# Optimization experiments

Measured on AMD Instinct MI355X. Metric: run time of the kernel, lower is better.

Reference implementation:

```python
import jax, jax.numpy as jnp
import numpy as np

N, G, H1, H2, HEADS, EMB, C, S = 4096, 2048, 512, 128, 8, 16, 20, 4
CH = H1 // HEADS  # per-head channels = 64
EPS = 1e-6
COEF_FE = 0.1


def _uni(k, shape, fan_in, fan_out):
    c = np.sqrt(6.0 / (fan_in + fan_out)).astype(np.float32)
    return jax.random.uniform(k, shape, jnp.float32, -c, c)


def setup_inputs() -> dict:
    key = jax.random.key(0)
    ks = jax.random.split(key, 40)
    adj = (jax.random.uniform(ks[0], (N, N)) < 0.005).astype(jnp.float32)
    adj = jnp.maximum(adj, jnp.eye(N, dtype=jnp.float32))  # self-loops, no empty rows
    node_feats = jax.random.normal(ks[1], (N, G), jnp.float32)
    count_matrix = jax.random.randint(ks[2], (N, G), 0, 50).astype(jnp.float32)
    library_size = jax.random.uniform(ks[3], (N, 1), jnp.float32, 0.5, 2.0)
    slice_label = jax.random.randint(ks[4], (N,), 0, S)
    basis = jax.random.uniform(ks[5], (C, G), jnp.float32)
    # encoder GAT layer1: HEADS heads, c_in=G -> c_out=CH each
    We1 = _uni(ks[6], (HEADS, CH, G), G, CH)
    be1 = jnp.zeros((HEADS, CH), jnp.float32)
    v0e1 = _uni(ks[7], (HEADS, CH, 1), CH, 1)
    v1e1 = _uni(ks[8], (HEADS, CH, 1), CH, 1)
    # encoder dense layer2: H1 -> H2
    W2 = _uni(ks[9], (H2, H1), H1, H2)
    b2 = jnp.zeros((H2,), jnp.float32)
    # decoder GAT layer1: c_in = H2+EMB -> CH per head
    CIN_D = H2 + EMB
    Wd1 = _uni(ks[10], (HEADS, CH, CIN_D), CIN_D, CH)
    bd1 = jnp.zeros((HEADS, CH), jnp.float32)
    v0d1 = _uni(ks[11], (HEADS, CH, 1), CH, 1)
    v1d1 = _uni(ks[12], (HEADS, CH, 1), CH, 1)
    # decoder dense layer2: H1 -> G
    Wd2 = _uni(ks[13], (G, H1), H1, G)
    bd2 = jnp.zeros((G,), jnp.float32)
    # deconv alpha (H2+EMB -> 1) and beta (H2 -> C); zero-init in torch, small random here
    Wa = 0.01 * jax.random.normal(ks[14], (1, CIN_D), jnp.float32)
    ba = jnp.zeros((1,), jnp.float32)
    Wb = 0.01 * jax.random.normal(ks[15], (C, H2), jnp.float32)
    bb = jnp.zeros((C,), jnp.float32)
    gamma = 0.01 * jax.random.normal(ks[16], (S, G), jnp.float32)
    logtheta = 5.0 * jnp.ones((S, G), jnp.float32)
    emb_table = jax.random.normal(ks[17], (S, EMB), jnp.float32)
    return dict(adj_matrix=adj, node_feats=node_feats, count_matrix=count_matrix,
                library_size=library_size, slice_label=slice_label, basis=basis,
                We1=We1, be1=be1, v0e1=v0e1, v1e1=v1e1, W2=W2, b2=b2,
                Wd1=Wd1, bd1=bd1, v0d1=v0d1, v1d1=v1d1, Wd2=Wd2, bd2=bd2,
                Wa=Wa, ba=ba, Wb=Wb, bb=bb, gamma=gamma, logtheta=logtheta,
                emb_table=emb_table)


def _gat_head(x, adj, W, b, v0, v1):
    h = x @ W.T + b                       # [N, CH]
    logits = adj * ((h @ v0) + (h @ v1).T)  # [N, N]; zero where adj==0
    s = jax.nn.sigmoid(logits) - 0.5       # unnormalized attentions
    mask = adj != 0.0
    e = jnp.where(mask, jnp.exp(s), 0.0)    # sparse softmax over structural nonzeros (temp=1)
    den = e.sum(axis=1, keepdims=True)
    p = e / jnp.where(den == 0.0, 1.0, den)
    return p @ h                            # [N, CH]


def _gat_multi(x, adj, Ws, bs, v0s, v1s):
    return jnp.concatenate([_gat_head(x, adj, Ws[i], bs[i], v0s[i], v1s[i])
                            for i in range(HEADS)], axis=1)


def reference(adj_matrix, node_feats, count_matrix, library_size, slice_label, basis,
              We1, be1, v0e1, v1e1, W2, b2, Wd1, bd1, v0d1, v1d1, Wd2, bd2,
              Wa, ba, Wb, bb, gamma, logtheta, emb_table):
    # encoder
    H = jax.nn.elu(_gat_multi(node_feats, adj_matrix, We1, be1, v0e1, v1e1))
    Z = H @ W2.T + b2                                   # [N, H2]
    emb = emb_table[slice_label]                        # [N, EMB]
    # deconvolutioner
    beta = jax.nn.softmax(jax.nn.elu(Z) @ Wb.T + bb, axis=1)   # [N, C]
    Hc = jax.nn.elu(jnp.concatenate([Z, emb], axis=1))
    alpha = Hc @ Wa.T + ba                              # [N, 1]
    # decoder
    Hd = jax.nn.elu(_gat_multi(jnp.concatenate([Z, emb], axis=1), adj_matrix,
                               Wd1, bd1, v0d1, v1d1))
    X_recon = Hd @ Wd2.T + bd2                          # [N, G]
    features_loss = jnp.mean(jnp.sqrt(jnp.sum((node_feats - X_recon) ** 2, axis=1)))
    # NB deconvolution loss
    log_lam = jnp.log(beta @ basis + EPS) + alpha + gamma[slice_label]
    lam = jnp.exp(log_lam)
    th = jnp.exp(logtheta)[slice_label]                 # [N, G]
    mu = library_size * lam
    ll = (jax.lax.lgamma(count_matrix + th + EPS) - jax.lax.lgamma(th + EPS)
          + th * jnp.log(th + EPS) - th * jnp.log(th + mu + EPS)
          + count_matrix * jnp.log(mu + EPS) - count_matrix * jnp.log(th + mu + EPS))
    decon_loss = -jnp.mean(jnp.sum(ll, axis=1))
    return decon_loss + COEF_FE * features_loss
```

## Files before the change

kernel.cpp:

```cpp
#include <hip/hip_runtime.h>
#include <hip/hip_bf16.h>
#include <math.h>

#define N 4096
#define G 2048
#define H1 512
#define H2 128
#define HEADS 8
#define EMB 16
#define C 20
#define S 4
#define CH 64
#define CIN_D (H2 + EMB)
#define KD_PAD 160
#define KB_PAD 32
#define CAP 128
#define EPSV 1e-6f

typedef __attribute__((ext_vector_type(8))) short short8;
typedef __attribute__((ext_vector_type(8))) short bf16x8;
typedef __attribute__((ext_vector_type(4))) float f32x4;

__device__ __forceinline__ unsigned short f2b(float x) {
    __hip_bfloat16 h = __float2bfloat16(x);
    return *reinterpret_cast<unsigned short*>(&h);
}
__device__ __forceinline__ float b2f(unsigned short u) {
    unsigned int x = ((unsigned int)u) << 16;
    return __uint_as_float(x);
}
__device__ __forceinline__ float lgamma_fast(float x) {
    float sh = 0.f;
    while (x < 8.f) { sh -= __logf(x); x += 1.f; }
    float ix = 1.f / x;
    float lx = __logf(x);
    return (x - 0.5f) * lx - x + 0.91893853f
         + ix * (0.08333333f - 0.00277778f * ix * ix) + sh;
}

#define SEG_SG   (S * G)
#define SEG_NF4  (N * G / 4)
#define SEG_WE4  (H1 * G / 4)
#define SEG_W24  (H2 * H1 / 4)
#define SEG_WD1E (H1 * KD_PAD)
#define SEG_WD24 (G * H1 / 4)
#define SEG_BTE  (G * KB_PAD)
#define PREP_TOTAL (SEG_SG + SEG_NF4 + SEG_WE4 + SEG_W24 + SEG_WD1E + SEG_WD24 + SEG_BTE)
#define CSR_BLOCKS (N / 4)
#define PREP_BLOCKS ((PREP_TOTAL + 255) / 256)

__device__ __forceinline__ void cvt4(const float* __restrict__ in,
                                     unsigned short* __restrict__ out, int i) {
    float4 v = ((const float4*)in)[i];
    ushort4 o;
    o.x = f2b(v.x); o.y = f2b(v.y); o.z = f2b(v.z); o.w = f2b(v.w);
    ((ushort4*)out)[i] = o;
}

__global__ __launch_bounds__(256) void csr_prep(const float* __restrict__ adj,
                                                int* __restrict__ col_idx,
                                                int* __restrict__ row_cnt,
                                                const float* __restrict__ logtheta,
                                                const float* __restrict__ gamma,
                                                float* __restrict__ th_a, float* __restrict__ eg_a,
                                                float* __restrict__ gm_a, float* __restrict__ ax_a,
                                                const float* __restrict__ node_f,
                                                unsigned short* __restrict__ nf_bf,
                                                const float* __restrict__ We1,
                                                unsigned short* __restrict__ We1_bf,
                                                const float* __restrict__ W2,
                                                unsigned short* __restrict__ W2_bf,
                                                const float* __restrict__ Wd1,
                                                unsigned short* __restrict__ Wd1_bf,
                                                const float* __restrict__ Wd2,
                                                unsigned short* __restrict__ Wd2_bf,
                                                const float* __restrict__ basis,
                                                unsigned short* __restrict__ basisT_bf) {
    int b = blockIdx.x;
    if (b < CSR_BLOCKS) {
        int wv = threadIdx.x >> 6, lane = threadIdx.x & 63;
        int i = b * 4 + wv;
        int cnt = 0;
        const float4* row4 = (const float4*)(adj + (size_t)i * N);
        int* cols = col_idx + (size_t)i * CAP;
        unsigned long long lmask = (1ull << lane) - 1ull;
        for (int c = 0; c < N / 256; ++c) {
            float4 v = row4[c * 64 + lane];
            float vv[4] = {v.x, v.y, v.z, v.w};
            #pragma unroll
            for (int s = 0; s < 4; ++s) {
                unsigned long long m = __ballot(vv[s] != 0.f);
                if (vv[s] != 0.f) {
                    int idx = cnt + __popcll(m & lmask);
                    if (idx < CAP) cols[idx] = c * 256 + lane * 4 + s;
                }
                cnt += __popcll(m);
            }
        }
        if (lane == 0) row_cnt[i] = cnt < CAP ? cnt : CAP;
        return;
    }
    int idx = (b - CSR_BLOCKS) * 256 + threadIdx.x;
    if (idx < SEG_SG) {
        float th = __expf(logtheta[idx]);
        float gm = gamma[idx];
        th_a[idx] = th;
        eg_a[idx] = __expf(gm);
        gm_a[idx] = gm;
        ax_a[idx] = th * __logf(th + EPSV) - lgammaf(th + EPSV);
        return;
    }
    idx -= SEG_SG;
    if (idx < SEG_NF4) { cvt4(node_f, nf_bf, idx); return; }
    idx -= SEG_NF4;
    if (idx < SEG_WE4) { cvt4(We1, We1_bf, idx); return; }
    idx -= SEG_WE4;
    if (idx < SEG_W24) { cvt4(W2, W2_bf, idx); return; }
    idx -= SEG_W24;
    if (idx < SEG_WD1E) {
        int n = idx / KD_PAD, k = idx - n * KD_PAD;
        Wd1_bf[idx] = f2b(k < CIN_D ? Wd1[n * CIN_D + k] : 0.f);
        return;
    }
    idx -= SEG_WD1E;
    if (idx < SEG_WD24) { cvt4(Wd2, Wd2_bf, idx); return; }
    idx -= SEG_WD24;
    if (idx < SEG_BTE) {
        int g = idx >> 5, c = idx & 31;
        basisT_bf[idx] = f2b(c < C ? basis[c * G + g] : 0.f);
    }
}

#define LDP 40
template<int FM, int OBF, int KS, int HV>
__global__ __launch_bounds__(256) void gemm_mfma(const unsigned short* __restrict__ A,
                                                 const unsigned short* __restrict__ B,
                                                 const float* __restrict__ bias,
                                                 void* __restrict__ Cout,
                                                 int M, int Nc, int K,
                                                 const float* __restrict__ v0f,
                                                 const float* __restrict__ v1f,
                                                 float* __restrict__ hv0,
                                                 float* __restrict__ hv1) {
    constexpr int BMT = FM * 32;
    __shared__ short As[BMT * LDP];
    __shared__ short Bs[128 * LDP];
    int bn = blockIdx.x, bm = blockIdx.y;
    int kz = (KS > 1) ? blockIdx.z : 0;
    int t = threadIdx.x;
    int lane = t & 63, wid = t >> 6;
    int wr = wid >> 1, wc = wid & 1;
    f32x4 acc[FM][4] = {};
    const short* Ag = (const short*)A + (size_t)(bm * BMT) * K;
    const short* Bg = (const short*)B + (size_t)(bn * 128) * K;
    int r0 = t >> 2, q0 = t & 3;
    int rbase = (lane & 15);
    int koff = (lane >> 4) * 8;
    int kbeg = kz * (K / KS), kend = kbeg + K / KS;

    for (int k0 = kbeg; k0 < kend; k0 += 32) {
        short8 a0 = *(const short8*)(Ag + (size_t)r0 * K + k0 + q0 * 8);
        short8 a1;
        if constexpr (FM == 4) a1 = *(const short8*)(Ag + (size_t)(r0 + 64) * K + k0 + q0 * 8);
        short8 b0 = *(const short8*)(Bg + (size_t)r0 * K + k0 + q0 * 8);
        short8 b1 = *(const short8*)(Bg + (size_t)(r0 + 64) * K + k0 + q0 * 8);
        __syncthreads();
        *(short8*)(As + r0 * LDP + q0 * 8) = a0;
        if constexpr (FM == 4) *(short8*)(As + (r0 + 64) * LDP + q0 * 8) = a1;
        *(short8*)(Bs + r0 * LDP + q0 * 8) = b0;
        *(short8*)(Bs + (r0 + 64) * LDP + q0 * 8) = b1;
        __syncthreads();
        bf16x8 af[FM], bfr[4];
        #pragma unroll
        for (int m = 0; m < FM; ++m)
            af[m] = *(const bf16x8*)(As + (wr * FM * 16 + m * 16 + rbase) * LDP + koff);
        #pragma unroll
        for (int n = 0; n < 4; ++n)
            bfr[n] = *(const bf16x8*)(Bs + (wc * 64 + n * 16 + rbase) * LDP + koff);
        #pragma unroll
        for (int m = 0; m < FM; ++m)
            #pragma unroll
            for (int n = 0; n < 4; ++n)
                acc[m][n] = __builtin_amdgcn_mfma_f32_16x16x32_bf16(af[m], bfr[n], acc[m][n], 0, 0, 0);
    }
    int colb = bn * 128 + wc * 64;
    int rowb = bm * BMT + wr * FM * 16;
    #pragma unroll
    for (int m = 0; m < FM; ++m) {
        #pragma unroll
        for (int n = 0; n < 4; ++n) {
            int col = colb + n * 16 + (lane & 15);
            int row0 = rowb + m * 16 + (lane >> 4) * 4;
            if constexpr (KS > 1) {
                float* Cp = (float*)Cout + (size_t)kz * M * Nc;
                #pragma unroll
                for (int r = 0; r < 4; ++r)
                    Cp[(size_t)(row0 + r) * Nc + col] = acc[m][n][r];
            } else {
                float bs = bias ? bias[col] : 0.f;
                #pragma unroll
                for (int r = 0; r < 4; ++r) {
                    float v = acc[m][n][r] + bs;
                    if constexpr (OBF)
                        ((unsigned short*)Cout)[(size_t)(row0 + r) * Nc + col] = f2b(v);
                    else
                        ((float*)Cout)[(size_t)(row0 + r) * Nc + col] = v;
                }
            }
        }
    }
    if constexpr (HV) {
        int h = colb >> 6;
        #pragma unroll
        for (int m = 0; m < FM; ++m) {
            #pragma unroll
            for (int r = 0; r < 4; ++r) {
                int row = rowb + m * 16 + (lane >> 4) * 4 + r;
                float p0 = 0.f, p1 = 0.f;
                #pragma unroll
                for (int n = 0; n < 4; ++n) {
                    int col = colb + n * 16 + (lane & 15);
                    float v = acc[m][n][r] + bias[col];
                    p0 += v * v0f[col];
                    p1 += v * v1f[col];
                }
                p0 += __shfl_xor(p0, 1); p0 += __shfl_xor(p0, 2);
                p0 += __shfl_xor(p0, 4); p0 += __shfl_xor(p0, 8);
                p1 += __shfl_xor(p1, 1); p1 += __shfl_xor(p1, 2);
                p1 += __shfl_xor(p1, 4); p1 += __shfl_xor(p1, 8);
                if ((lane & 15) == 0) {
                    hv0[row * HEADS + h] = p0;
                    hv1[row * HEADS + h] = p1;
                }
            }
        }
    }
}

template<int HV>
__device__ __forceinline__ void gemm_body2(const unsigned short* __restrict__ A,
                                           const unsigned short* __restrict__ B,
                                           const float* __restrict__ bias,
                                           unsigned short* __restrict__ Cout,
                                           int K, int Nc, int bn, int bm,
                                           const float* __restrict__ v0f,
                                           const float* __restrict__ v1f,
                                           float* __restrict__ hv0,
                                           float* __restrict__ hv1,
                                           short* As, short* Bs) {
    int t = threadIdx.x;
    int lane = t & 63, wid = t >> 6;
    int wr = wid >> 1, wc = wid & 1;
    f32x4 acc[2][4] = {};
    const short* Ag = (const short*)A + (size_t)(bm * 64) * K;
    const short* Bg = (const short*)B + (size_t)(bn * 128) * K;
    int r0 = t >> 2, q0 = t & 3;
    int rbase = (lane & 15);
    int koff = (lane >> 4) * 8;
    for (int k0 = 0; k0 < K; k0 += 32) {
        short8 a0 = *(const short8*)(Ag + (size_t)r0 * K + k0 + q0 * 8);
        short8 b0 = *(const short8*)(Bg + (size_t)r0 * K + k0 + q0 * 8);
        short8 b1 = *(const short8*)(Bg + (size_t)(r0 + 64) * K + k0 + q0 * 8);
        __syncthreads();
        *(short8*)(As + r0 * LDP + q0 * 8) = a0;
        *(short8*)(Bs + r0 * LDP + q0 * 8) = b0;
        *(short8*)(Bs + (r0 + 64) * LDP + q0 * 8) = b1;
        __syncthreads();
        bf16x8 af[2], bfr[4];
        #pragma unroll
        for (int m = 0; m < 2; ++m)
            af[m] = *(const bf16x8*)(As + (wr * 32 + m * 16 + rbase) * LDP + koff);
        #pragma unroll
        for (int n = 0; n < 4; ++n)
            bfr[n] = *(const bf16x8*)(Bs + (wc * 64 + n * 16 + rbase) * LDP + koff);
        #pragma unroll
        for (int m = 0; m < 2; ++m)
            #pragma unroll
            for (int n = 0; n < 4; ++n)
                acc[m][n] = __builtin_amdgcn_mfma_f32_16x16x32_bf16(af[m], bfr[n], acc[m][n], 0, 0, 0);
    }
    int colb = bn * 128 + wc * 64;
    int rowb = bm * 64 + wr * 32;
    #pragma unroll
    for (int m = 0; m < 2; ++m) {
        #pragma unroll
        for (int n = 0; n < 4; ++n) {
            int col = colb + n * 16 + (lane & 15);
            int row0 = rowb + m * 16 + (lane >> 4) * 4;
            float bs = bias ? bias[col] : 0.f;
            #pragma unroll
            for (int r = 0; r < 4; ++r)
                Cout[(size_t)(row0 + r) * Nc + col] = f2b(acc[m][n][r] + bs);
        }
    }
    if constexpr (HV) {
        int h = colb >> 6;
        #pragma unroll
        for (int m = 0; m < 2; ++m) {
            #pragma unroll
            for (int r = 0; r < 4; ++r) {
                int row = rowb + m * 16 + (lane >> 4) * 4 + r;
                float p0 = 0.f, p1 = 0.f;
                #pragma unroll
                for (int n = 0; n < 4; ++n) {
                    int col = colb + n * 16 + (lane & 15);
                    float v = acc[m][n][r] + bias[col];
                    p0 += v * v0f[col];
                    p1 += v * v1f[col];
                }
                p0 += __shfl_xor(p0, 1); p0 += __shfl_xor(p0, 2);
                p0 += __shfl_xor(p0, 4); p0 += __shfl_xor(p0, 8);
                p1 += __shfl_xor(p1, 1); p1 += __shfl_xor(p1, 2);
                p1 += __shfl_xor(p1, 4); p1 += __shfl_xor(p1, 8);
                if ((lane & 15) == 0) {
                    hv0[row * HEADS + h] = p0;
                    hv1[row * HEADS + h] = p1;
                }
            }
        }
    }
}

__global__ __launch_bounds__(256) void dec_bd(const unsigned short* __restrict__ Xd_bf,
                                              const unsigned short* __restrict__ Wd1_bf,
                                              const float* __restrict__ bd1,
                                              unsigned short* __restrict__ Hlin_bf,
                                              const float* __restrict__ v0d1,
                                              const float* __restrict__ v1d1,
                                              float* __restrict__ hv0,
                                              float* __restrict__ hv1,
                                              const unsigned short* __restrict__ beta_bf,
                                              const unsigned short* __restrict__ basisT_bf,
                                              unsigned short* __restrict__ BDb) {
    __shared__ short As[64 * LDP];
    __shared__ short Bs[128 * LDP];
    int b = blockIdx.x;
    if (b < (H1 / 128) * (N / 64)) {
        gemm_body2<1>(Xd_bf, Wd1_bf, bd1, Hlin_bf, KD_PAD, H1,
                      b % (H1 / 128), b / (H1 / 128), v0d1, v1d1, hv0, hv1, As, Bs);
    } else {
        int b2 = b - (H1 / 128) * (N / 64);
        gemm_body2<0>(beta_bf, basisT_bf, nullptr, BDb, KB_PAD, G,
                      b2 % (G / 128), b2 / (G / 128), nullptr, nullptr, nullptr, nullptr, As, Bs);
    }
}

template<int KS>
__global__ __launch_bounds__(256) void reduce_k_hv(const float* __restrict__ Cp,
                                                   const float* __restrict__ bias,
                                                   unsigned short* __restrict__ out,
                                                   const float* __restrict__ v0f,
                                                   const float* __restrict__ v1f,
                                                   float* __restrict__ hv0,
                                                   float* __restrict__ hv1) {
    constexpr int total4 = N * H1 / 4;
    int t = threadIdx.x;
    int i = blockIdx.x * 256 + t;
    float4 s = ((const float4*)Cp)[i];
    #pragma unroll
    for (int ks = 1; ks < KS; ++ks) {
        float4 v = ((const float4*)(Cp + (size_t)ks * total4 * 4))[i];
        s.x += v.x; s.y += v.y; s.z += v.z; s.w += v.w;
    }
    int col = (i * 4) & (H1 - 1);
    s.x += bias[col]; s.y += bias[col + 1]; s.z += bias[col + 2]; s.w += bias[col + 3];
    ushort4 o;
    o.x = f2b(s.x); o.y = f2b(s.y); o.z = f2b(s.z); o.w = f2b(s.w);
    ((ushort4*)out)[i] = o;
    int row = (i * 4) >> 9;
    int h = col >> 6;
    float4 w0 = *(const float4*)(v0f + col);
    float4 w1 = *(const float4*)(v1f + col);
    float p0 = s.x * w0.x + s.y * w0.y + s.z * w0.z + s.w * w0.w;
    float p1 = s.x * w1.x + s.y * w1.y + s.z * w1.z + s.w * w1.w;
    p0 += __shfl_xor(p0, 1); p0 += __shfl_xor(p0, 2);
    p0 += __shfl_xor(p0, 4); p0 += __shfl_xor(p0, 8);
    p1 += __shfl_xor(p1, 1); p1 += __shfl_xor(p1, 2);
    p1 += __shfl_xor(p1, 4); p1 += __shfl_xor(p1, 8);
    if ((t & 15) == 0) {
        hv0[row * HEADS + h] = p0;
        hv1[row * HEADS + h] = p1;
    }
}

__global__ __launch_bounds__(256) void z_pernode(const float* __restrict__ Cp,
                                                 const float* __restrict__ b2,
                                                 const float* __restrict__ emb_table,
                                                 const int* __restrict__ slab,
                                                 const float* __restrict__ Wb,
                                                 const float* __restrict__ bb,
                                                 const float* __restrict__ Wa,
                                                 const float* __restrict__ ba,
                                                 const float* __restrict__ lib,
                                                 unsigned short* __restrict__ beta_bf,
                                                 float* __restrict__ muf,
                                                 float* __restrict__ kco,
                                                 unsigned short* __restrict__ Xdb) {
    __shared__ float sZ[4][H2];
    __shared__ float sE[4][EMB];
    __shared__ float sLog[4][C];
    __shared__ float sAl[4];
    int wv = threadIdx.x >> 6;
    int lane = threadIdx.x & 63;
    int i = blockIdx.x * 4 + wv;
    float z0 = 0.f, z1 = 0.f;
    #pragma unroll
    for (int ks = 0; ks < 8; ++ks) {
        const float* P = Cp + (size_t)ks * N * H2 + (size_t)i * H2;
        z0 += P[lane];
        z1 += P[64 + lane];
    }
    z0 += b2[lane];
    z1 += b2[64 + lane];
    sZ[wv][lane] = z0;
    sZ[wv][64 + lane] = z1;
    int s = slab[i];
    if (lane < EMB) sE[wv][lane] = emb_table[s * EMB + lane];
    __syncthreads();
    Xdb[(size_t)i * KD_PAD + lane] = f2b(z0);
    Xdb[(size_t)i * KD_PAD + 64 + lane] = f2b(z1);
    if (lane < EMB) Xdb[(size_t)i * KD_PAD + H2 + lane] = f2b(sE[wv][lane]);
    if (lane < KD_PAD - CIN_D) Xdb[(size_t)i * KD_PAD + CIN_D + lane] = 0;
    if (lane < C) {
        float acc = bb[lane];
        for (int k = 0; k < H2; ++k) {
            float z = sZ[wv][k];
            float e = z > 0.f ? z : expm1f(z);
            acc += e * Wb[lane * H2 + k];
        }
        sLog[wv][lane] = acc;
    }
    __syncthreads();
    if (lane == 0) {
        float mx = sLog[wv][0];
        for (int c = 1; c < C; ++c) mx = fmaxf(mx, sLog[wv][c]);
        float sm = 0.f;
        for (int c = 0; c < C; ++c) { float e = __expf(sLog[wv][c] - mx); sLog[wv][c] = e; sm += e; }
        for (int c = 0; c < C; ++c) sLog[wv][c] /= sm;
    }
    __syncthreads();
    if (lane < KB_PAD) beta_bf[(size_t)i * KB_PAD + lane] = (lane < C) ? f2b(sLog[wv][lane]) : 0;
    float x0 = z0; x0 = x0 > 0.f ? x0 : expm1f(x0);
    float x1 = z1; x1 = x1 > 0.f ? x1 : expm1f(x1);
    float p = x0 * Wa[lane] + x1 * Wa[64 + lane];
    if (lane < EMB) {
        float x2 = sE[wv][lane]; x2 = x2 > 0.f ? x2 : expm1f(x2);
        p += x2 * Wa[H2 + lane];
    }
    #pragma unroll
    for (int m = 32; m; m >>= 1) p += __shfl_xor(p, m);
    if (lane == 0) sAl[wv] = p + ba[0];
    __syncthreads();
    if (lane == 0) {
        float A = sAl[wv], L = lib[i];
        muf[i] = L * __expf(A);
        kco[i] = __logf(L) + A;
    }
}

__global__ __launch_bounds__(256) void gemm_recon_sq(const unsigned short* __restrict__ A,
                                                     const unsigned short* __restrict__ B,
                                                     const float* __restrict__ bias,
                                                     const unsigned short* __restrict__ nfb,
                                                     float* __restrict__ sq_part) {
    constexpr int K = H1;
    __shared__ short As[64 * LDP];
    __shared__ short Bs[128 * LDP];
    __shared__ float red[4][32];
    int bn = blockIdx.x, bm = blockIdx.y;
    int t = threadIdx.x;
    int lane = t & 63, wid = t >> 6;
    int wr = wid >> 1, wc = wid & 1;
    f32x4 acc[2][4] = {};
    const short* Ag = (const short*)A + (size_t)(bm * 64) * K;
    const short* Bg = (const short*)B + (size_t)(bn * 128) * K;
    int r0 = t >> 2, q0 = t & 3;
    int rbase = (lane & 15);
    int koff = (lane >> 4) * 8;

    for (int k0 = 0; k0 < K; k0 += 32) {
        short8 a0 = *(const short8*)(Ag + (size_t)r0 * K + k0 + q0 * 8);
        short8 b0 = *(const short8*)(Bg + (size_t)r0 * K + k0 + q0 * 8);
        short8 b1 = *(const short8*)(Bg + (size_t)(r0 + 64) * K + k0 + q0 * 8);
        __syncthreads();
        *(short8*)(As + r0 * LDP + q0 * 8) = a0;
        *(short8*)(Bs + r0 * LDP + q0 * 8) = b0;
        *(short8*)(Bs + (r0 + 64) * LDP + q0 * 8) = b1;
        __syncthreads();
        bf16x8 af[2], bfr[4];
        #pragma unroll
        for (int m = 0; m < 2; ++m)
            af[m] = *(const bf16x8*)(As + (wr * 32 + m * 16 + rbase) * LDP + koff);
        #pragma unroll
        for (int n = 0; n < 4; ++n)
            bfr[n] = *(const bf16x8*)(Bs + (wc * 64 + n * 16 + rbase) * LDP + koff);
        #pragma unroll
        for (int m = 0; m < 2; ++m)
            #pragma unroll
            for (int n = 0; n < 4; ++n)
                acc[m][n] = __builtin_amdgcn_mfma_f32_16x16x32_bf16(af[m], bfr[n], acc[m][n], 0, 0, 0);
    }
    int colb = bn * 128 + wc * 64;
    int rowb = bm * 64 + wr * 32;
    float part[2][4];
    #pragma unroll
    for (int m = 0; m < 2; ++m) {
        #pragma unroll
        for (int r = 0; r < 4; ++r) part[m][r] = 0.f;
        #pragma unroll
        for (int n = 0; n < 4; ++n) {
            int col = colb + n * 16 + (lane & 15);
            float bs = bias[col];
            int row0 = rowb + m * 16 + (lane >> 4) * 4;
            #pragma unroll
            for (int r = 0; r < 4; ++r) {
                float d = b2f(nfb[(size_t)(row0 + r) * G + col]) - (acc[m][n][r] + bs);
                part[m][r] += d * d;
            }
        }
    }
    #pragma unroll
    for (int m = 0; m < 2; ++m)
        #pragma unroll
        for (int r = 0; r < 4; ++r) {
            float v = part[m][r];
            v += __shfl_xor(v, 1); v += __shfl_xor(v, 2);
            v += __shfl_xor(v, 4); v += __shfl_xor(v, 8);
            part[m][r] = v;
        }
    if ((lane & 15) == 0) {
        int q = lane >> 4;
        #pragma unroll
        for (int m = 0; m < 2; ++m)
            #pragma unroll
            for (int r = 0; r < 4; ++r)
                red[wid][m * 16 + q * 4 + r] = part[m][r];
    }
    __syncthreads();
    if (t < 64) {
        int wr2 = t >> 5, loc = t & 31;
        float v = red[wr2 * 2 + 0][loc] + red[wr2 * 2 + 1][loc];
        sq_part[(size_t)(bm * 64 + t) * 16 + bn] = v;
    }
}

__global__ __launch_bounds__(256) void nb_loss_ew(const unsigned short* __restrict__ BDb,
                                                  const float* __restrict__ cm,
                                                  const int* __restrict__ slab,
                                                  const float* __restrict__ muf,
                                                  const float* __restrict__ kco,
                                                  const float* __restrict__ th_a,
                                                  const float* __restrict__ eg_a,
                                                  const float* __restrict__ gm_a,
                                                  const float* __restrict__ ax_a,
                                                  float* __restrict__ ll_row) {
    int row = blockIdx.x * 4 + (threadIdx.x >> 6);
    int lane = threadIdx.x & 63;
    int sl = slab[row];
    float mufv = muf[row], kcov = kco[row];
    const unsigned short* bdr = BDb + (size_t)row * G;
    const float* cmr = cm + (size_t)row * G;
    size_t sgb = (size_t)sl * G;
    float acc = 0.f;
    #pragma unroll 2
    for (int it = 0; it < G / 256; ++it) {
        int c = it * 256 + lane * 4;
        ushort4 bdu = *(const ushort4*)(bdr + c);
        f32x4 k4  = *(const f32x4*)(cmr + c);
        f32x4 th4 = *(const f32x4*)(th_a + sgb + c);
        f32x4 eg4 = *(const f32x4*)(eg_a + sgb + c);
        f32x4 gm4 = *(const f32x4*)(gm_a + sgb + c);
        f32x4 ax4 = *(const f32x4*)(ax_a + sgb + c);
        float bdv[4] = {b2f(bdu.x), b2f(bdu.y), b2f(bdu.z), b2f(bdu.w)};
        #pragma unroll
        for (int j = 0; j < 4; ++j) {
            float th = th4[j], k = k4[j];
            float ebd = bdv[j] + EPSV;
            float lbd = __logf(ebd);
            float mu = mufv * ebd * eg4[j];
            float lgx = lgamma_fast(k + th + EPSV);
            acc += lgx + ax4[j] - (th + k) * __logf(th + mu + EPSV)
                 + k * (kcov + lbd + gm4[j]);
        }
    }
    #pragma unroll
    for (int m = 32; m; m >>= 1) acc += __shfl_xor(acc, m);
    if (lane == 0) ll_row[row] = acc;
}

__global__ __launch_bounds__(512) void attn_fused(const unsigned short* __restrict__ Hb,
                                                  const float* __restrict__ hv0,
                                                  const float* __restrict__ hv1,
                                                  const int* __restrict__ col_idx,
                                                  const int* __restrict__ row_cnt,
                                                  unsigned short* __restrict__ out) {
    __shared__ int scols[CAP];
    __shared__ float sw[CAP][HEADS];
    __shared__ float sden[HEADS];
    __shared__ float red[8][64 * 8];
    int i = blockIdx.x;
    int t = threadIdx.x;
    int cnt = row_cnt[i];
    const int* cols = col_idx + (size_t)i * CAP;
    if (t < cnt) scols[t] = cols[t];
    __syncthreads();
    for (int idx = t; idx < cnt * HEADS; idx += 512) {
        int e = idx >> 3, h = idx & 7;
        int j = scols[e];
        float x = hv0[i * HEADS + h] + hv1[j * HEADS + h];
        sw[e][h] = __expf(1.f / (1.f + __expf(-x)) - 0.5f);
    }
    __syncthreads();
    if (t < HEADS) {
        float d = 0.f;
        for (int e = 0; e < cnt; ++e) d += sw[e][t];
        sden[t] = 1.f / d;
    }
    __syncthreads();
    int slot = t >> 6;
    int cg = t & 63;
    int h = cg >> 3;
    float inv = sden[h];
    float acc[8];
    #pragma unroll
    for (int k = 0; k < 8; ++k) acc[k] = 0.f;
    for (int e = slot; e < cnt; e += 8) {
        int j = scols[e];
        float wv = sw[e][h] * inv;
        short8 hv = ((const short8*)(Hb + (size_t)j * H1))[cg];
        #pragma unroll
        for (int k = 0; k < 8; ++k)
            acc[k] += wv * b2f((unsigned short)hv[k]);
    }
    #pragma unroll
    for (int k = 0; k < 8; ++k) red[slot][cg * 8 + k] = acc[k];
    __syncthreads();
    if (slot < 4) {
        #pragma unroll
        for (int k = 0; k < 8; ++k) red[slot][cg * 8 + k] += red[slot + 4][cg * 8 + k];
    }
    __syncthreads();
    if (slot < 2) {
        #pragma unroll
        for (int k = 0; k < 8; ++k) red[slot][cg * 8 + k] += red[slot + 2][cg * 8 + k];
    }
    __syncthreads();
    if (slot == 0) {
        short8 o;
        #pragma unroll
        for (int k = 0; k < 8; ++k) {
            float v = red[0][cg * 8 + k] + red[1][cg * 8 + k];
            v = (v > 0.f) ? v : expm1f(v);
            o[k] = (short)f2b(v);
        }
        ((short8*)(out + (size_t)i * H1))[cg] = o;
    }
}

__global__ __launch_bounds__(256) void final_reduce(const float* __restrict__ ll_row,
                                                    const float* __restrict__ sq_part,
                                                    float* __restrict__ out) {
    int t = threadIdx.x;
    float s1 = 0.f, sb = 0.f;
    for (int row = t; row < N; row += 256) {
        s1 += ll_row[row];
        float s2 = 0.f;
        #pragma unroll
        for (int j = 0; j < 16; ++j) s2 += sq_part[(size_t)row * 16 + j];
        sb += sqrtf(s2);
    }
    __shared__ float r1[256], r2[256];
    r1[t] = s1; r2[t] = sb;
    __syncthreads();
    for (int o = 128; o; o >>= 1) {
        if (t < o) { r1[t] += r1[t + o]; r2[t] += r2[t + o]; }
        __syncthreads();
    }
    if (t == 0) out[0] = -(r1[0] / (float)N) + 0.1f * (r2[0] / (float)N);
}

extern "C" void kernel_launch(void* const* d_in, const int* in_sizes, int n_in,
                              void* d_out, int out_size, void* d_ws, size_t ws_size,
                              hipStream_t stream) {
    const float* adj       = (const float*)d_in[0];
    const float* node_f    = (const float*)d_in[1];
    const float* count_m   = (const float*)d_in[2];
    const float* lib       = (const float*)d_in[3];
    const int*   slab      = (const int*)d_in[4];
    const float* basis     = (const float*)d_in[5];
    const float* We1       = (const float*)d_in[6];
    const float* be1       = (const float*)d_in[7];
    const float* v0e1      = (const float*)d_in[8];
    const float* v1e1      = (const float*)d_in[9];
    const float* W2        = (const float*)d_in[10];
    const float* b2        = (const float*)d_in[11];
    const float* Wd1       = (const float*)d_in[12];
    const float* bd1       = (const float*)d_in[13];
    const float* v0d1      = (const float*)d_in[14];
    const float* v1d1      = (const float*)d_in[15];
    const float* Wd2       = (const float*)d_in[16];
    const float* bd2       = (const float*)d_in[17];
    const float* Wa        = (const float*)d_in[18];
    const float* ba        = (const float*)d_in[19];
    const float* Wb        = (const float*)d_in[20];
    const float* bb        = (const float*)d_in[21];
    const float* gamma     = (const float*)d_in[22];
    const float* logtheta  = (const float*)d_in[23];
    const float* emb_table = (const float*)d_in[24];
    float* out = (float*)d_out;

    char* w = (char*)d_ws;
    auto alloc = [&](size_t bytes) { void* p = (void*)w; w += (bytes + 255) & ~(size_t)255; return p; };
    int*   col_idx = (int*)  alloc((size_t)N * CAP * 4);
    int*   row_cnt = (int*)  alloc((size_t)N * 4);
    unsigned short* Hlin_bf = (unsigned short*)alloc((size_t)N * H1 * 2);
    unsigned short* Hgat_bf = (unsigned short*)alloc((size_t)N * H1 * 2);
    unsigned short* Xd_bf   = (unsigned short*)alloc((size_t)N * KD_PAD * 2);
    unsigned short* beta_bf = (unsigned short*)alloc((size_t)N * KB_PAD * 2);
    float* muf     = (float*)alloc((size_t)N * 4);
    float* kco     = (float*)alloc((size_t)N * 4);
    float* hv0     = (float*)alloc((size_t)N * HEADS * 4);
    float* hv1     = (float*)alloc((size_t)N * HEADS * 4);
    float* th_a    = (float*)alloc((size_t)S * G * 4);
    float* eg_a    = (float*)alloc((size_t)S * G * 4);
    float* gm_a    = (float*)alloc((size_t)S * G * 4);
    float* ax_a    = (float*)alloc((size_t)S * G * 4);
    float* Cp      = (float*)alloc((size_t)4 * N * H1 * 4);
    unsigned short* BDb = (unsigned short*)alloc((size_t)N * G * 2);
    float* ll_row  = (float*)alloc((size_t)N * 4);
    float* sq_part = (float*)alloc((size_t)N * 16 * 4);
    unsigned short* nf_bf    = (unsigned short*)alloc((size_t)N * G * 2);
    unsigned short* We1_bf   = (unsigned short*)alloc((size_t)H1 * G * 2);
    unsigned short* W2_bf    = (unsigned short*)alloc((size_t)H2 * H1 * 2);
    unsigned short* Wd1_bf   = (unsigned short*)alloc((size_t)H1 * KD_PAD * 2);
    unsigned short* Wd2_bf   = (unsigned short*)alloc((size_t)G * H1 * 2);
    unsigned short* basisT_bf= (unsigned short*)alloc((size_t)G * KB_PAD * 2);

    csr_prep<<<dim3(CSR_BLOCKS + PREP_BLOCKS), dim3(256), 0, stream>>>(
        adj, col_idx, row_cnt, logtheta, gamma, th_a, eg_a, gm_a, ax_a,
        node_f, nf_bf, We1, We1_bf, W2, W2_bf, Wd1, Wd1_bf, Wd2, Wd2_bf, basis, basisT_bf);

    gemm_mfma<2, 0, 4, 0><<<dim3(H1 / 128, N / 64, 4), dim3(256), 0, stream>>>(
        nf_bf, We1_bf, be1, Cp, N, H1, G, nullptr, nullptr, nullptr, nullptr);
    reduce_k_hv<4><<<dim3(N * H1 / 4 / 256), dim3(256), 0, stream>>>(
        Cp, be1, Hlin_bf, v0e1, v1e1, hv0, hv1);
    attn_fused<<<dim3(N), dim3(512), 0, stream>>>(Hlin_bf, hv0, hv1, col_idx, row_cnt, Hgat_bf);
    gemm_mfma<2, 0, 8, 0><<<dim3(H2 / 128, N / 64, 8), dim3(256), 0, stream>>>(
        Hgat_bf, W2_bf, b2, Cp, N, H2, H1, nullptr, nullptr, nullptr, nullptr);
    z_pernode<<<dim3(N / 4), dim3(256), 0, stream>>>(
        Cp, b2, emb_table, slab, Wb, bb, Wa, ba, lib, beta_bf, muf, kco, Xd_bf);
    dec_bd<<<dim3((H1 / 128) * (N / 64) + (G / 128) * (N / 64)), dim3(256), 0, stream>>>(
        Xd_bf, Wd1_bf, bd1, Hlin_bf, v0d1, v1d1, hv0, hv1, beta_bf, basisT_bf, BDb);
    nb_loss_ew<<<dim3(N / 4), dim3(256), 0, stream>>>(
        BDb, count_m, slab, muf, kco, th_a, eg_a, gm_a, ax_a, ll_row);
    attn_fused<<<dim3(N), dim3(512), 0, stream>>>(Hlin_bf, hv0, hv1, col_idx, row_cnt, Hgat_bf);
    gemm_recon_sq<<<dim3(G / 128, N / 64), dim3(256), 0, stream>>>(
        Hgat_bf, Wd2_bf, bd2, nf_bf, sq_part);
    final_reduce<<<dim3(1), dim3(256), 0, stream>>>(ll_row, sq_part, out);
}
```

Measured before the change: 185.7 us.

## Fuse decoder attention with NB loss kernel and rewrite CSR extraction

Merges the second attention kernel and the NB loss elementwise kernel into one launch, with block ranges split between the two independent workloads so they run concurrently and one launch is saved. The CSR build now has each lane scan a contiguous 64-column chunk into a bitmask, then uses a wave prefix scan to place column indices. This replaces the per-element ballot loop. The cost is that the NB blocks now run 512 threads each while also carrying the attention kernel's shared-memory footprint, which may lower occupancy. The new CSR reads are strided per lane, which may hurt load coalescing.

```diff
diff --git a/kernel.cpp b/kernel.cpp
--- a/kernel.cpp
+++ b/kernel.cpp
@@ -80,24 +80,34 @@
     if (b < CSR_BLOCKS) {
         int wv = threadIdx.x >> 6, lane = threadIdx.x & 63;
         int i = b * 4 + wv;
-        int cnt = 0;
         const float4* row4 = (const float4*)(adj + (size_t)i * N);
+        unsigned long long mask = 0ull;
+        #pragma unroll
+        for (int q = 0; q < 16; ++q) {
+            float4 v = row4[lane * 16 + q];
+            if (v.x != 0.f) mask |= 1ull << (q * 4 + 0);
+            if (v.y != 0.f) mask |= 1ull << (q * 4 + 1);
+            if (v.z != 0.f) mask |= 1ull << (q * 4 + 2);
+            if (v.w != 0.f) mask |= 1ull << (q * 4 + 3);
+        }
+        int cnt = __popcll(mask);
+        int incl = cnt;
+        #pragma unroll
+        for (int off = 1; off < 64; off <<= 1) {
+            int v = __shfl_up(incl, off);
+            if (lane >= off) incl += v;
+        }
+        int ofs = incl - cnt;
+        int total = __shfl(incl, 63);
         int* cols = col_idx + (size_t)i * CAP;
-        unsigned long long lmask = (1ull << lane) - 1ull;
-        for (int c = 0; c < N / 256; ++c) {
-            float4 v = row4[c * 64 + lane];
-            float vv[4] = {v.x, v.y, v.z, v.w};
-            #pragma unroll
-            for (int s = 0; s < 4; ++s) {
-                unsigned long long m = __ballot(vv[s] != 0.f);
-                if (vv[s] != 0.f) {
-                    int idx = cnt + __popcll(m & lmask);
-                    if (idx < CAP) cols[idx] = c * 256 + lane * 4 + s;
-                }
-                cnt += __popcll(m);
-            }
-        }
-        if (lane == 0) row_cnt[i] = cnt < CAP ? cnt : CAP;
+        unsigned long long mm = mask;
+        while (mm) {
+            int j = __ffsll(mm) - 1;
+            if (ofs < CAP) cols[ofs] = lane * 64 + j;
+            ++ofs;
+            mm &= mm - 1;
+        }
+        if (lane == 0) row_cnt[i] = total < CAP ? total : CAP;
         return;
     }
     int idx = (b - CSR_BLOCKS) * 256 + threadIdx.x;
@@ -544,18 +554,17 @@
     }
 }
 
-__global__ __launch_bounds__(256) void nb_loss_ew(const unsigned short* __restrict__ BDb,
-                                                  const float* __restrict__ cm,
-                                                  const int* __restrict__ slab,
-                                                  const float* __restrict__ muf,
-                                                  const float* __restrict__ kco,
-                                                  const float* __restrict__ th_a,
-                                                  const float* __restrict__ eg_a,
-                                                  const float* __restrict__ gm_a,
-                                                  const float* __restrict__ ax_a,
-                                                  float* __restrict__ ll_row) {
-    int row = blockIdx.x * 4 + (threadIdx.x >> 6);
-    int lane = threadIdx.x & 63;
+__device__ __forceinline__ void nb_row_body(int row, int lane,
+                                            const unsigned short* __restrict__ BDb,
+                                            const float* __restrict__ cm,
+                                            const int* __restrict__ slab,
+                                            const float* __restrict__ muf,
+                                            const float* __restrict__ kco,
+                                            const float* __restrict__ th_a,
+                                            const float* __restrict__ eg_a,
+                                            const float* __restrict__ gm_a,
+                                            const float* __restrict__ ax_a,
+                                            float* __restrict__ ll_row) {
     int sl = slab[row];
     float mufv = muf[row], kcov = kco[row];
     const unsigned short* bdr = BDb + (size_t)row * G;
@@ -588,72 +597,106 @@
     if (lane == 0) ll_row[row] = acc;
 }
 
+__device__ __forceinline__ void attn_body(int i, int t,
+                                          const unsigned short* __restrict__ Hb,
+                                          const float* __restrict__ hv0,
+                                          const float* __restrict__ hv1,
+                                          const int* __restrict__ col_idx,
+                                          const int* __restrict__ row_cnt,
+                                          unsigned short* __restrict__ outp) {
+    __shared__ int scols[CAP];
+    __shared__ float sw[CAP][HEADS];
+    __shared__ float sden[HEADS];
+    __shared__ float red[8][64 * 8];
+    int cnt = row_cnt[i];
+    const int* cols = col_idx + (size_t)i * CAP;
+    if (t < cnt) scols[t] = cols[t];
+    __syncthreads();
+    for (int idx = t; idx < cnt * HEADS; idx += 512) {
+        int e = idx >> 3, h = idx & 7;
+        int j = scols[e];
+        float x = hv0[i * HEADS + h] + hv1[j * HEADS + h];
+        sw[e][h] = __expf(1.f / (1.f + __expf(-x)) - 0.5f);
+    }
+    __syncthreads();
+    if (t < HEADS) {
+        float d = 0.f;
+        for (int e = 0; e < cnt; ++e) d += sw[e][t];
+        sden[t] = 1.f / d;
+    }
+    __syncthreads();
+    int slot = t >> 6;
+    int cg = t & 63;
+    int h = cg >> 3;
+    float inv = sden[h];
+    float acc[8];
+    #pragma unroll
+    for (int k = 0; k < 8; ++k) acc[k] = 0.f;
+    for (int e = slot; e < cnt; e += 8) {
+        int j = scols[e];
+        float wv = sw[e][h] * inv;
+        short8 hvv = ((const short8*)(Hb + (size_t)j * H1))[cg];
+        #pragma unroll
+        for (int k = 0; k < 8; ++k)
+            acc[k] += wv * b2f((unsigned short)hvv[k]);
+    }
+    #pragma unroll
+    for (int k = 0; k < 8; ++k) red[slot][cg * 8 + k] = acc[k];
+    __syncthreads();
+    if (slot < 4) {
+        #pragma unroll
+        for (int k = 0; k < 8; ++k) red[slot][cg * 8 + k] += red[slot + 4][cg * 8 + k];
+    }
+    __syncthreads();
+    if (slot < 2) {
+        #pragma unroll
+        for (int k = 0; k < 8; ++k) red[slot][cg * 8 + k] += red[slot + 2][cg * 8 + k];
+    }
+    __syncthreads();
+    if (slot == 0) {
+        short8 o;
+        #pragma unroll
+        for (int k = 0; k < 8; ++k) {
+            float v = red[0][cg * 8 + k] + red[1][cg * 8 + k];
+            v = (v > 0.f) ? v : expm1f(v);
+            o[k] = (short)f2b(v);
+        }
+        ((short8*)(outp + (size_t)i * H1))[cg] = o;
+    }
+}
+
 __global__ __launch_bounds__(512) void attn_fused(const unsigned short* __restrict__ Hb,
                                                   const float* __restrict__ hv0,
                                                   const float* __restrict__ hv1,
                                                   const int* __restrict__ col_idx,
                                                   const int* __restrict__ row_cnt,
                                                   unsigned short* __restrict__ out) {
-    __shared__ int scols[CAP];
-    __shared__ float sw[CAP][HEADS];
-    __shared__ float sden[HEADS];
-    __shared__ float red[8][64 * 8];
-    int i = blockIdx.x;
-    int t = threadIdx.x;
-    int cnt = row_cnt[i];
-    const int* cols = col_idx + (size_t)i * CAP;
-    if (t < cnt) scols[t] = cols[t];
-    __syncthreads();
-    for (int idx = t; idx < cnt * HEADS; idx += 512) {
-        int e = idx >> 3, h = idx & 7;
-        int j = scols[e];
-        float x = hv0[i * HEADS + h] + hv1[j * HEADS + h];
-        sw[e][h] = __expf(1.f / (1.f + __expf(-x)) - 0.5f);
-    }
-    __syncthreads();
-    if (t < HEADS) {
-        float d = 0.f;
-        for (int e = 0; e < cnt; ++e) d += sw[e][t];
-        sden[t] = 1.f / d;
-    }
-    __syncthreads();
-    int slot = t >> 6;
-    int cg = t & 63;
-    int h = cg >> 3;
-    float inv = sden[h];
-    float acc[8];
-    #pragma unroll
-    for (int k = 0; k < 8; ++k) acc[k] = 0.f;
-    for (int e = slot; e < cnt; e += 8) {
-        int j = scols[e];
-        float wv = sw[e][h] * inv;
-        short8 hv = ((const short8*)(Hb + (size_t)j * H1))[cg];
-        #pragma unroll
-        for (int k = 0; k < 8; ++k)
-            acc[k] += wv * b2f((unsigned short)hv[k]);
-    }
-    #pragma unroll
-    for (int k = 0; k < 8; ++k) red[slot][cg * 8 + k] = acc[k];
-    __syncthreads();
-    if (slot < 4) {
-        #pragma unroll
-        for (int k = 0; k < 8; ++k) red[slot][cg * 8 + k] += red[slot + 4][cg * 8 + k];
-    }
-    __syncthreads();
-    if (slot < 2) {
-        #pragma unroll
-        for (int k = 0; k < 8; ++k) red[slot][cg * 8 + k] += red[slot + 2][cg * 8 + k];
-    }
-    __syncthreads();
-    if (slot == 0) {
-        short8 o;
-        #pragma unroll
-        for (int k = 0; k < 8; ++k) {
-            float v = red[0][cg * 8 + k] + red[1][cg * 8 + k];
-            v = (v > 0.f) ? v : expm1f(v);
-            o[k] = (short)f2b(v);
-        }
-        ((short8*)(out + (size_t)i * H1))[cg] = o;
+    attn_body(blockIdx.x, threadIdx.x, Hb, hv0, hv1, col_idx, row_cnt, out);
+}
+
+__global__ __launch_bounds__(512) void post_dec(const unsigned short* __restrict__ Hlin_bf,
+                                                const float* __restrict__ hv0,
+                                                const float* __restrict__ hv1,
+                                                const int* __restrict__ col_idx,
+                                                const int* __restrict__ row_cnt,
+                                                unsigned short* __restrict__ Hgat_bf,
+                                                const unsigned short* __restrict__ BDb,
+                                                const float* __restrict__ cm,
+                                                const int* __restrict__ slab,
+                                                const float* __restrict__ muf,
+                                                const float* __restrict__ kco,
+                                                const float* __restrict__ th_a,
+                                                const float* __restrict__ eg_a,
+                                                const float* __restrict__ gm_a,
+                                                const float* __restrict__ ax_a,
+                                                float* __restrict__ ll_row) {
+    int b = blockIdx.x;
+    if (b < N) {
+        attn_body(b, threadIdx.x, Hlin_bf, hv0, hv1, col_idx, row_cnt, Hgat_bf);
+    } else {
+        int row = (b - N) * 8 + (threadIdx.x >> 6);
+        nb_row_body(row, threadIdx.x & 63, BDb, cm, slab, muf, kco,
+                    th_a, eg_a, gm_a, ax_a, ll_row);
     }
 }
 
@@ -751,9 +794,9 @@
         Cp, b2, emb_table, slab, Wb, bb, Wa, ba, lib, beta_bf, muf, kco, Xd_bf);
     dec_bd<<<dim3((H1 / 128) * (N / 64) + (G / 128) * (N / 64)), dim3(256), 0, stream>>>(
         Xd_bf, Wd1_bf, bd1, Hlin_bf, v0d1, v1d1, hv0, hv1, beta_bf, basisT_bf, BDb);
-    nb_loss_ew<<<dim3(N / 4), dim3(256), 0, stream>>>(
+    post_dec<<<dim3(N + N / 8), dim3(512), 0, stream>>>(
+        Hlin_bf, hv0, hv1, col_idx, row_cnt, Hgat_bf,
         BDb, count_m, slab, muf, kco, th_a, eg_a, gm_a, ax_a, ll_row);
-    attn_fused<<<dim3(N), dim3(512), 0, stream>>>(Hlin_bf, hv0, hv1, col_idx, row_cnt, Hgat_bf);
     gemm_recon_sq<<<dim3(G / 128, N / 64), dim3(256), 0, stream>>>(
         Hgat_bf, Wd2_bf, bd2, nf_bf, sq_part);
     final_reduce<<<dim3(1), dim3(256), 0, stream>>>(ll_row, sq_part, out);
```

After: 201.0 us. 8.3% more time.
